# Kernel tuning notes

Hardware: AMD Instinct MI355X
Metric: run time of the kernel (lower is better)

Reference implementation:

```python
import jax, jax.numpy as jnp
import numpy as np

B, D, H, NC = 4096, 128, 4, 10
HD = D // H
EPS = 1e-5


def _ln(x, g, b):
    m = jnp.mean(x, axis=-1, keepdims=True)
    v = jnp.var(x, axis=-1, keepdims=True)
    return (x - m) * jax.lax.rsqrt(v + EPS) * g + b


def _mlp(x, w1, b1, w2, b2):
    h = jax.nn.gelu(x @ w1.T + b1, approximate=False)  # nn.GELU default = exact erf
    return h @ w2.T + b2


def setup_inputs():
    key = jax.random.key(0)
    ks = iter(jax.random.split(key, 40))
    w = lambda *s: jax.random.normal(next(ks), s, dtype=jnp.float32) * 0.02
    inp = {
        'coords': jax.random.uniform(next(ks), (B, 2), dtype=jnp.float32),
        'labels': jax.random.randint(next(ks), (B,), 0, NC),
        'ce_w': w(D, 2), 'ce_b': w(D),
        'emb': w(NC, D),
        'sa_in_w': w(3 * D, D), 'sa_in_b': w(3 * D),
        'sa_out_w': w(D, D), 'sa_out_b': w(D),
        'n1_g': jnp.ones(D), 'n1_b': jnp.zeros(D),
        'm1_w1': w(4 * D, D), 'm1_b1': w(4 * D), 'm1_w2': w(D, 4 * D), 'm1_b2': w(D),
        'n2_g': jnp.ones(D), 'n2_b': jnp.zeros(D),
        'ca_in_w': w(3 * D, D), 'ca_in_b': w(3 * D),
        'ca_out_w': w(D, D), 'ca_out_b': w(D),
        'n3_g': jnp.ones(D), 'n3_b': jnp.zeros(D),
        'm2_w1': w(4 * D, D), 'm2_b1': w(4 * D), 'm2_w2': w(D, 4 * D), 'm2_b2': w(D),
        'n4_g': jnp.ones(D), 'n4_b': jnp.zeros(D),
        'fin_w': w(1, D), 'fin_b': w(1),
    }
    return inp


def reference(coords, labels, ce_w, ce_b, emb, sa_in_w, sa_in_b, sa_out_w, sa_out_b,
              n1_g, n1_b, m1_w1, m1_b1, m1_w2, m1_b2, n2_g, n2_b,
              ca_in_w, ca_in_b, ca_out_w, ca_out_b, n3_g, n3_b,
              m2_w1, m2_b1, m2_w2, m2_b2, n4_g, n4_b, fin_w, fin_b):
    # --- vectorized positional encoding (original loops over batch) ---
    div = 10000.0 ** (2.0 * jnp.arange(D // 2, dtype=jnp.float32) / D)  # [D/2]
    pe_sin = jnp.sin(coords[:, 0:1] / div)  # even slots
    pe_cos = jnp.cos(coords[:, 1:2] / div)  # odd slots
    pe = jnp.stack([pe_sin, pe_cos], axis=-1).reshape(B, D)

    x = coords @ ce_w.T + ce_b + pe  # [B, D]

    # --- self-attention: seq_len = B, batch = 1 (torch seq-first semantics) ---
    qkv = x @ sa_in_w.T + sa_in_b  # [B, 3D]
    q, k, v = jnp.split(qkv, 3, axis=-1)
    q = q.reshape(B, H, HD); k = k.reshape(B, H, HD); v = v.reshape(B, H, HD)
    scores = jnp.einsum('qhd,khd->hqk', q, k) / jnp.sqrt(jnp.float32(HD))  # [H,B,B]
    attn = jax.nn.softmax(scores, axis=-1)
    sa = jnp.einsum('hqk,khd->qhd', attn, v).reshape(B, D) @ sa_out_w.T + sa_out_b

    x = _ln(x + sa, n1_g, n1_b)
    x = _ln(x + _mlp(x, m1_w1, m1_b1, m1_w2, m1_b2), n2_g, n2_b)

    # --- cross-attention: per-sample q_len = kv_len = 1 -> softmax over a
    # single key is exactly 1, so output = out_proj(v_proj(label_emb)) ---
    lab = emb[labels]  # [B, D]
    wv = ca_in_w[2 * D:]; bv = ca_in_b[2 * D:]
    ca = (lab @ wv.T + bv) @ ca_out_w.T + ca_out_b

    x = _ln(x + ca, n3_g, n3_b)
    x = _ln(x + _mlp(x, m2_w1, m2_b1, m2_w2, m2_b2), n4_g, n4_b)

    return jax.nn.sigmoid(x @ fin_w.T + fin_b)  # [B, 1]
```

## Files before the change

### kernel.cpp

```cpp
#include <hip/hip_runtime.h>
#include <hip/hip_bf16.h>


typedef __bf16 bf16_t;
typedef __bf16 bf16x8 __attribute__((ext_vector_type(8)));
typedef __bf16 bf16x4 __attribute__((ext_vector_type(4)));
typedef __bf16 bf16x2 __attribute__((ext_vector_type(2)));
typedef float  f32x4  __attribute__((ext_vector_type(4)));
typedef float  f32x2  __attribute__((ext_vector_type(2)));

__device__ __forceinline__ f32x4 mfma16(bf16x8 a, bf16x8 b, f32x4 c) {
  return __builtin_amdgcn_mfma_f32_16x16x32_bf16(a, b, c, 0, 0, 0);
}

__global__ __launch_bounds__(256) void k_init(const float* __restrict__ coords,
                                              const float* __restrict__ ce_w,
                                              const float* __restrict__ ce_b,
                                              float* __restrict__ xf,
                                              bf16_t* __restrict__ xb,
                                              const float* __restrict__ s0,
                                              const float* __restrict__ s1,
                                              const float* __restrict__ s2,
                                              const float* __restrict__ s3,
                                              const float* __restrict__ s4,
                                              const float* __restrict__ s5,
                                              bf16_t* __restrict__ wdst,
                                              const float* __restrict__ emb,
                                              const float* __restrict__ wvp,
                                              const float* __restrict__ bvp,
                                              const float* __restrict__ cow,
                                              const float* __restrict__ cob,
                                              float* __restrict__ tab) {
  const int bid = blockIdx.x;
  const int tid = threadIdx.x;
  if (bid < 2048) {
    int row = bid * 2 + (tid >> 7);
    int d   = tid & 127;
    float c0 = coords[row * 2 + 0];
    float c1 = coords[row * 2 + 1];
    int   j  = d >> 1;
    float inv = exp2f(-0.20762050593045953f * (float)j);
    float pe  = (d & 1) ? cosf(c1 * inv) : sinf(c0 * inv);
    float x = c0 * ce_w[2 * d] + c1 * ce_w[2 * d + 1] + ce_b[d] + pe;
    xf[(size_t)row * 128 + d] = x;
    xb[(size_t)row * 128 + d] = (bf16_t)x;
  } else if (bid < 2368) {
    int i = (bid - 2048) * 256 + tid;
    const float* src; int off;
    if      (i < 12288) { src = s0; off = i; }
    else if (i < 16384) { src = s1; off = i - 12288; }
    else if (i < 32768) { src = s2; off = i - 16384; }
    else if (i < 49152) { src = s3; off = i - 32768; }
    else if (i < 65536) { src = s4; off = i - 49152; }
    else                { src = s5; off = i - 65536; }
    f32x4 v = *(const f32x4*)(src + (size_t)off * 4);
    bf16x4 o = {(bf16_t)v[0], (bf16_t)v[1], (bf16_t)v[2], (bf16_t)v[3]};
    *(bf16x4*)(wdst + (size_t)i * 4) = o;
  } else {
    __shared__ float embs[10][128];
    __shared__ float t1[10][128];
    for (int i = tid; i < 1280; i += 256) embs[i >> 7][i & 127] = emb[i];
    __syncthreads();
    for (int o = tid; o < 1280; o += 256) {
      int c = o >> 7, n = o & 127;
      float acc = bvp[n];
      const float* wr = wvp + n * 128;
      for (int k2 = 0; k2 < 128; k2++) acc += embs[c][k2] * wr[k2];
      t1[c][n] = acc;
    }
    __syncthreads();
    for (int o = tid; o < 1280; o += 256) {
      int c = o >> 7, dd = o & 127;
      float acc = cob[dd];
      const float* wr = cow + dd * 128;
      for (int n = 0; n < 128; n++) acc += t1[c][n] * wr[n];
      tab[o] = acc;
    }
  }
}

enum { EPI_BF16 = 1, EPI_GELU_BF16 = 2 };

template <int K, int EPI>
__global__ __launch_bounds__(256) void k_gemm(const bf16_t* __restrict__ X,
                                              const bf16_t* __restrict__ Wb,
                                              const float* __restrict__ bias,
                                              bf16_t* __restrict__ outB,
                                              bf16_t* __restrict__ vTout,
                                              int N) {
  const int tid  = threadIdx.x;
  const int lane = tid & 63;
  const int wv   = tid >> 6;
  const int l15  = lane & 15;
  const int quad = lane >> 4;
  const int xbase = blockIdx.x * 64 + (wv >> 1) * 32;
  const int wbase = blockIdx.y * 64 + (wv & 1) * 32;

  const bf16_t* wr0 = Wb + (size_t)(wbase + l15) * K + quad * 8;
  const bf16_t* xr0 = X  + (size_t)(xbase + l15) * K + quad * 8;

  f32x4 acc[2][2];
  const f32x4 zero4 = {0.f, 0.f, 0.f, 0.f};
  for (int i = 0; i < 2; i++)
    for (int t = 0; t < 2; t++) acc[i][t] = zero4;

#pragma unroll 4
  for (int kk = 0; kk < K; kk += 32) {
    bf16x8 a0 = *(const bf16x8*)(wr0 + kk);
    bf16x8 a1 = *(const bf16x8*)(wr0 + 16 * K + kk);
    bf16x8 b0 = *(const bf16x8*)(xr0 + kk);
    bf16x8 b1 = *(const bf16x8*)(xr0 + 16 * K + kk);
    acc[0][0] = mfma16(a0, b0, acc[0][0]);
    acc[0][1] = mfma16(a0, b1, acc[0][1]);
    acc[1][0] = mfma16(a1, b0, acc[1][0]);
    acc[1][1] = mfma16(a1, b1, acc[1][1]);
  }

  f32x4 bv[2];
  bv[0] = *(const f32x4*)(bias + wbase + quad * 4);
  bv[1] = *(const f32x4*)(bias + wbase + 16 + quad * 4);
#pragma unroll
  for (int t = 0; t < 2; t++) {
    int row = xbase + t * 16 + l15;
#pragma unroll
    for (int i = 0; i < 2; i++) {
      int col0 = wbase + i * 16 + quad * 4;
      f32x4 v = acc[i][t] + bv[i];
      if (EPI == EPI_GELU_BF16) {
#pragma unroll
        for (int r = 0; r < 4; r++)
          v[r] = 0.5f * v[r] * (1.0f + erff(v[r] * 0.70710678118654752f));
      }
      bf16x4 o = {(bf16_t)v[0], (bf16_t)v[1], (bf16_t)v[2], (bf16_t)v[3]};
      *(bf16x4*)(outB + (size_t)row * N + col0) = o;
      if (vTout && col0 >= 256) {
#pragma unroll
        for (int r = 0; r < 4; r++)
          vTout[(size_t)(col0 - 256 + r) * 4096 + row] = (bf16_t)v[r];
      }
    }
  }
}

__global__ __launch_bounds__(256, 4) void k_attn(const bf16_t* __restrict__ qkv,
                                                 const bf16_t* __restrict__ vT,
                                                 bf16_t* __restrict__ opart,
                                                 float* __restrict__ lpart) {
  __shared__ bf16_t kbuf[128][36];
  __shared__ bf16_t vbuf[32][136];
  __shared__ bf16_t pt[4][2][16][72];

  const int tid  = threadIdx.x;
  const int lane = tid & 63;
  const int wv   = tid >> 6;
  const int l15  = lane & 15;
  const int quad = lane >> 4;
  const int blk  = blockIdx.x;
  const int h    = blk & 3;
  const int ks   = (blk >> 2) & 7;
  const int qt   = (blk >> 5) * 4 + wv;
  const int q0   = qt * 32;
  const int kb   = ks * 512;
  const int task = (qt * 8 + ks) * 4 + h;

  bf16x8 qfA, qfB;
  {
    bf16x8 ra = *(const bf16x8*)(qkv + (size_t)(q0 + l15) * 384 + h * 32 + quad * 8);
    bf16x8 rb = *(const bf16x8*)(qkv + (size_t)(q0 + 16 + l15) * 384 + h * 32 + quad * 8);
#pragma unroll
    for (int j = 0; j < 8; j++) {
      qfA[j] = (bf16_t)((float)ra[j] * 0.17677669529663687f);
      qfB[j] = (bf16_t)((float)rb[j] * 0.17677669529663687f);
    }
  }

  const f32x4 zero4 = {0.f, 0.f, 0.f, 0.f};
  f32x4 oA0 = zero4, oA1 = zero4, oB0 = zero4, oB1 = zero4;
  float laccA = 0.f, laccB = 0.f;

  for (int kk = 0; kk < 512; kk += 128) {
    __syncthreads();
#pragma unroll
    for (int rep = 0; rep < 2; rep++) {
      int idx = rep * 256 + tid;
      int row = idx >> 2, seg = idx & 3;
      bf16x8 t8 = *(const bf16x8*)(qkv + (size_t)(kb + kk + row) * 384
                                   + 128 + h * 32 + seg * 8);
      *(bf16x8*)&kbuf[row][seg * 8] = t8;
      int dim = idx >> 4, vseg = idx & 15;
      bf16x8 v8 = *(const bf16x8*)(vT + (size_t)(h * 32 + dim) * 4096
                                   + kb + kk + vseg * 8);
      *(bf16x8*)&vbuf[dim][vseg * 8] = v8;
    }
    __syncthreads();

#pragma unroll
    for (int half = 0; half < 2; half++) {
      const int ko = half * 64;
      bf16x8 kf0 = *(const bf16x8*)&kbuf[ko + l15][quad * 8];
      bf16x8 kf1 = *(const bf16x8*)&kbuf[ko + 16 + l15][quad * 8];
      bf16x8 kf2 = *(const bf16x8*)&kbuf[ko + 32 + l15][quad * 8];
      bf16x8 kf3 = *(const bf16x8*)&kbuf[ko + 48 + l15][quad * 8];

      f32x4 sA[4], sB[4];
      sA[0] = mfma16(kf0, qfA, zero4);
      sA[1] = mfma16(kf1, qfA, zero4);
      sA[2] = mfma16(kf2, qfA, zero4);
      sA[3] = mfma16(kf3, qfA, zero4);
      sB[0] = mfma16(kf0, qfB, zero4);
      sB[1] = mfma16(kf1, qfB, zero4);
      sB[2] = mfma16(kf2, qfB, zero4);
      sB[3] = mfma16(kf3, qfB, zero4);

#pragma unroll
      for (int t = 0; t < 4; t++) {
        float a0 = __expf(sA[t][0]), a1 = __expf(sA[t][1]);
        float a2 = __expf(sA[t][2]), a3 = __expf(sA[t][3]);
        laccA += (a0 + a1) + (a2 + a3);
        bf16x4 pa = {(bf16_t)a0, (bf16_t)a1, (bf16_t)a2, (bf16_t)a3};
        *(bf16x4*)&pt[wv][0][l15][t * 16 + quad * 4] = pa;
        float b0 = __expf(sB[t][0]), b1 = __expf(sB[t][1]);
        float b2 = __expf(sB[t][2]), b3 = __expf(sB[t][3]);
        laccB += (b0 + b1) + (b2 + b3);
        bf16x4 pb = {(bf16_t)b0, (bf16_t)b1, (bf16_t)b2, (bf16_t)b3};
        *(bf16x4*)&pt[wv][1][l15][t * 16 + quad * 4] = pb;
      }

      bf16x8 pA0 = *(const bf16x8*)&pt[wv][0][l15][quad * 8];
      bf16x8 pA1 = *(const bf16x8*)&pt[wv][0][l15][32 + quad * 8];
      bf16x8 pB0 = *(const bf16x8*)&pt[wv][1][l15][quad * 8];
      bf16x8 pB1 = *(const bf16x8*)&pt[wv][1][l15][32 + quad * 8];

      bf16x8 v00 = *(const bf16x8*)&vbuf[l15][ko + quad * 8];
      bf16x8 v01 = *(const bf16x8*)&vbuf[16 + l15][ko + quad * 8];
      bf16x8 v10 = *(const bf16x8*)&vbuf[l15][ko + 32 + quad * 8];
      bf16x8 v11 = *(const bf16x8*)&vbuf[16 + l15][ko + 32 + quad * 8];

      oA0 = mfma16(pA0, v00, oA0);
      oA0 = mfma16(pA1, v10, oA0);
      oA1 = mfma16(pA0, v01, oA1);
      oA1 = mfma16(pA1, v11, oA1);
      oB0 = mfma16(pB0, v00, oB0);
      oB0 = mfma16(pB1, v10, oB0);
      oB1 = mfma16(pB0, v01, oB1);
      oB1 = mfma16(pB1, v11, oB1);
    }
  }

  laccA += __shfl_xor(laccA, 16, 64); laccA += __shfl_xor(laccA, 32, 64);
  laccB += __shfl_xor(laccB, 16, 64); laccB += __shfl_xor(laccB, 32, 64);
  if (quad == 0) {
    lpart[task * 32 + l15]      = laccA;
    lpart[task * 32 + 16 + l15] = laccB;
  }

  size_t ob = (size_t)task * 1024;
#pragma unroll
  for (int r = 0; r < 4; r++) {
    int qa = quad * 4 + r;
    opart[ob + qa * 32 + l15]             = (bf16_t)oA0[r];
    opart[ob + qa * 32 + 16 + l15]        = (bf16_t)oA1[r];
    opart[ob + (16 + qa) * 32 + l15]      = (bf16_t)oB0[r];
    opart[ob + (16 + qa) * 32 + 16 + l15] = (bf16_t)oB1[r];
  }
}

__global__ __launch_bounds__(256) void k_attn_fin(const bf16_t* __restrict__ opart,
                                                  const float* __restrict__ lpart,
                                                  bf16_t* __restrict__ attnb) {
  int idx = blockIdx.x * 256 + threadIdx.x;
  int d  = idx & 31;
  int q  = (idx >> 5) & 4095;
  int h  = idx >> 17;
  int qt = q >> 5, ql = q & 31;
  float O = 0.f, L = 0.f;
#pragma unroll
  for (int ks = 0; ks < 8; ks++) {
    int t = (qt * 8 + ks) * 4 + h;
    O += (float)opart[(size_t)t * 1024 + ql * 32 + d];
    L += lpart[t * 32 + ql];
  }
  attnb[(size_t)q * 128 + h * 32 + d] = (bf16_t)(O / L);
}

__global__ __launch_bounds__(512) void k_tail(
    const bf16_t* __restrict__ attnb, const float* __restrict__ xf,
    const bf16_t* __restrict__ wso, const float* __restrict__ bso,
    const float* __restrict__ n1g, const float* __restrict__ n1b,
    const bf16_t* __restrict__ w11, const float* __restrict__ b11,
    const bf16_t* __restrict__ w12, const float* __restrict__ b12,
    const float* __restrict__ n2g, const float* __restrict__ n2b,
    const int* __restrict__ labels, const float* __restrict__ tab,
    const float* __restrict__ n3g, const float* __restrict__ n3b,
    const bf16_t* __restrict__ w21, const float* __restrict__ b21,
    const bf16_t* __restrict__ w22, const float* __restrict__ b22,
    const float* __restrict__ n4g, const float* __restrict__ n4b,
    const float* __restrict__ fw, const float* __restrict__ fb,
    float* __restrict__ out) {
  __shared__ float  xs[16][132];
  __shared__ bf16_t xsb[16][136];
  __shared__ bf16_t hb[16][520];
  __shared__ float  red[2][16][8];

  const int tid  = threadIdx.x;
  const int lane = tid & 63;
  const int wv   = tid >> 6;
  const int l15  = lane & 15;
  const int quad = lane >> 4;
  const int row  = blockIdx.x * 16 + l15;
  const int cb1  = wv * 16;
  const int c1   = cb1 + quad * 4;
  const int cb4  = wv * 64;

  const f32x4 zero4 = {0.f, 0.f, 0.f, 0.f};

  {
    f32x4 acc = zero4;
    const bf16_t* br = attnb + (size_t)row * 128 + quad * 8;
    const bf16_t* ar = wso + (size_t)(cb1 + l15) * 128 + quad * 8;
#pragma unroll
    for (int kk = 0; kk < 128; kk += 32)
      acc = mfma16(*(const bf16x8*)(ar + kk), *(const bf16x8*)(br + kk), acc);

    f32x4 v = acc + *(const f32x4*)(bso + c1)
                  + *(const f32x4*)(xf + (size_t)row * 128 + c1);
    float s  = (v[0] + v[1]) + (v[2] + v[3]);
    float sq = (v[0]*v[0] + v[1]*v[1]) + (v[2]*v[2] + v[3]*v[3]);
    s  += __shfl_xor(s, 16, 64);  s  += __shfl_xor(s, 32, 64);
    sq += __shfl_xor(sq, 16, 64); sq += __shfl_xor(sq, 32, 64);
    if (quad == 0) { red[0][l15][wv] = s; red[1][l15][wv] = sq; }
    __syncthreads();
    float S = 0.f, SQ = 0.f;
#pragma unroll
    for (int w2 = 0; w2 < 8; w2++) { S += red[0][l15][w2]; SQ += red[1][l15][w2]; }
    float mean = S * (1.f / 128.f);
    float rstd = rsqrtf(SQ * (1.f / 128.f) - mean * mean + 1e-5f);
    f32x4 y = (v - mean) * rstd * (*(const f32x4*)(n1g + c1))
            + *(const f32x4*)(n1b + c1);
    *(f32x4*)&xs[l15][c1] = y;
    bf16x4 o = {(bf16_t)y[0], (bf16_t)y[1], (bf16_t)y[2], (bf16_t)y[3]};
    *(bf16x4*)&xsb[l15][c1] = o;
  }
  __syncthreads();

  {
    f32x4 au[4] = {zero4, zero4, zero4, zero4};
#pragma unroll
    for (int kk = 0; kk < 128; kk += 32) {
      bf16x8 bfr = *(const bf16x8*)&xsb[l15][kk + quad * 8];
#pragma unroll
      for (int i = 0; i < 4; i++) {
        bf16x8 a = *(const bf16x8*)(w11 + (size_t)(cb4 + i * 16 + l15) * 128
                                    + kk + quad * 8);
        au[i] = mfma16(a, bfr, au[i]);
      }
    }
#pragma unroll
    for (int i = 0; i < 4; i++) {
      int c = cb4 + i * 16 + quad * 4;
      f32x4 vv = au[i] + *(const f32x4*)(b11 + c);
#pragma unroll
      for (int r = 0; r < 4; r++)
        vv[r] = 0.5f * vv[r] * (1.0f + erff(vv[r] * 0.70710678118654752f));
      bf16x4 o = {(bf16_t)vv[0], (bf16_t)vv[1], (bf16_t)vv[2], (bf16_t)vv[3]};
      *(bf16x4*)&hb[l15][c] = o;
    }
  }
  __syncthreads();

  {
    f32x4 acc = zero4;
    const bf16_t* ar = w12 + (size_t)(cb1 + l15) * 512 + quad * 8;
#pragma unroll 4
    for (int kk = 0; kk < 512; kk += 32) {
      bf16x8 bfr = *(const bf16x8*)&hb[l15][kk + quad * 8];
      acc = mfma16(*(const bf16x8*)(ar + kk), bfr, acc);
    }
    f32x4 v = acc + *(const f32x4*)(b12 + c1) + *(const f32x4*)&xs[l15][c1];
    float s  = (v[0] + v[1]) + (v[2] + v[3]);
    float sq = (v[0]*v[0] + v[1]*v[1]) + (v[2]*v[2] + v[3]*v[3]);
    s  += __shfl_xor(s, 16, 64);  s  += __shfl_xor(s, 32, 64);
    sq += __shfl_xor(sq, 16, 64); sq += __shfl_xor(sq, 32, 64);
    if (quad == 0) { red[0][l15][wv] = s; red[1][l15][wv] = sq; }
    __syncthreads();
    float S = 0.f, SQ = 0.f;
#pragma unroll
    for (int w2 = 0; w2 < 8; w2++) { S += red[0][l15][w2]; SQ += red[1][l15][w2]; }
    float mean = S * (1.f / 128.f);
    float rstd = rsqrtf(SQ * (1.f / 128.f) - mean * mean + 1e-5f);
    int lab = labels[row];
    f32x4 y = (v - mean) * rstd * (*(const f32x4*)(n2g + c1))
            + *(const f32x4*)(n2b + c1)
            + *(const f32x4*)(tab + (size_t)lab * 128 + c1);
    float s3  = (y[0] + y[1]) + (y[2] + y[3]);
    float sq3 = (y[0]*y[0] + y[1]*y[1]) + (y[2]*y[2] + y[3]*y[3]);
    s3  += __shfl_xor(s3, 16, 64);  s3  += __shfl_xor(s3, 32, 64);
    sq3 += __shfl_xor(sq3, 16, 64); sq3 += __shfl_xor(sq3, 32, 64);
    __syncthreads();
    if (quad == 0) { red[0][l15][wv] = s3; red[1][l15][wv] = sq3; }
    __syncthreads();
    float S3 = 0.f, SQ3 = 0.f;
#pragma unroll
    for (int w2 = 0; w2 < 8; w2++) { S3 += red[0][l15][w2]; SQ3 += red[1][l15][w2]; }
    float mean3 = S3 * (1.f / 128.f);
    float rstd3 = rsqrtf(SQ3 * (1.f / 128.f) - mean3 * mean3 + 1e-5f);
    f32x4 y3 = (y - mean3) * rstd3 * (*(const f32x4*)(n3g + c1))
             + *(const f32x4*)(n3b + c1);
    *(f32x4*)&xs[l15][c1] = y3;
    bf16x4 o = {(bf16_t)y3[0], (bf16_t)y3[1], (bf16_t)y3[2], (bf16_t)y3[3]};
    *(bf16x4*)&xsb[l15][c1] = o;
  }
  __syncthreads();

  {
    f32x4 au[4] = {zero4, zero4, zero4, zero4};
#pragma unroll
    for (int kk = 0; kk < 128; kk += 32) {
      bf16x8 bfr = *(const bf16x8*)&xsb[l15][kk + quad * 8];
#pragma unroll
      for (int i = 0; i < 4; i++) {
        bf16x8 a = *(const bf16x8*)(w21 + (size_t)(cb4 + i * 16 + l15) * 128
                                    + kk + quad * 8);
        au[i] = mfma16(a, bfr, au[i]);
      }
    }
#pragma unroll
    for (int i = 0; i < 4; i++) {
      int c = cb4 + i * 16 + quad * 4;
      f32x4 vv = au[i] + *(const f32x4*)(b21 + c);
#pragma unroll
      for (int r = 0; r < 4; r++)
        vv[r] = 0.5f * vv[r] * (1.0f + erff(vv[r] * 0.70710678118654752f));
      bf16x4 o = {(bf16_t)vv[0], (bf16_t)vv[1], (bf16_t)vv[2], (bf16_t)vv[3]};
      *(bf16x4*)&hb[l15][c] = o;
    }
  }
  __syncthreads();

  {
    f32x4 acc = zero4;
    const bf16_t* ar = w22 + (size_t)(cb1 + l15) * 512 + quad * 8;
#pragma unroll 4
    for (int kk = 0; kk < 512; kk += 32) {
      bf16x8 bfr = *(const bf16x8*)&hb[l15][kk + quad * 8];
      acc = mfma16(*(const bf16x8*)(ar + kk), bfr, acc);
    }
    f32x4 v = acc + *(const f32x4*)(b22 + c1) + *(const f32x4*)&xs[l15][c1];
    float s  = (v[0] + v[1]) + (v[2] + v[3]);
    float sq = (v[0]*v[0] + v[1]*v[1]) + (v[2]*v[2] + v[3]*v[3]);
    s  += __shfl_xor(s, 16, 64);  s  += __shfl_xor(s, 32, 64);
    sq += __shfl_xor(sq, 16, 64); sq += __shfl_xor(sq, 32, 64);
    if (quad == 0) { red[0][l15][wv] = s; red[1][l15][wv] = sq; }
    __syncthreads();
    float S = 0.f, SQ = 0.f;
#pragma unroll
    for (int w2 = 0; w2 < 8; w2++) { S += red[0][l15][w2]; SQ += red[1][l15][w2]; }
    float mean = S * (1.f / 128.f);
    float rstd = rsqrtf(SQ * (1.f / 128.f) - mean * mean + 1e-5f);
    f32x4 y = (v - mean) * rstd * (*(const f32x4*)(n4g + c1))
            + *(const f32x4*)(n4b + c1);
    f32x4 fwv = *(const f32x4*)(fw + c1);
    float dot = (y[0]*fwv[0] + y[1]*fwv[1]) + (y[2]*fwv[2] + y[3]*fwv[3]);
    dot += __shfl_xor(dot, 16, 64); dot += __shfl_xor(dot, 32, 64);
    __syncthreads();
    if (quad == 0) red[0][l15][wv] = dot;
    __syncthreads();
    if (wv == 0 && quad == 0) {
      float logit = fb[0];
#pragma unroll
      for (int w2 = 0; w2 < 8; w2++) logit += red[0][l15][w2];
      out[row] = 1.0f / (1.0f + expf(-logit));
    }
  }
}

extern "C" void kernel_launch(void* const* d_in, const int* in_sizes, int n_in,
                              void* d_out, int out_size, void* d_ws, size_t ws_size,
                              hipStream_t stream) {
  const float* coords  = (const float*)d_in[0];
  const int*   labels  = (const int*)d_in[1];
  const float* ce_w    = (const float*)d_in[2];
  const float* ce_b    = (const float*)d_in[3];
  const float* emb     = (const float*)d_in[4];
  const float* sa_in_w = (const float*)d_in[5];
  const float* sa_in_b = (const float*)d_in[6];
  const float* sa_out_w= (const float*)d_in[7];
  const float* sa_out_b= (const float*)d_in[8];
  const float* n1_g    = (const float*)d_in[9];
  const float* n1_b    = (const float*)d_in[10];
  const float* m1_w1   = (const float*)d_in[11];
  const float* m1_b1   = (const float*)d_in[12];
  const float* m1_w2   = (const float*)d_in[13];
  const float* m1_b2   = (const float*)d_in[14];
  const float* n2_g    = (const float*)d_in[15];
  const float* n2_b    = (const float*)d_in[16];
  const float* ca_in_w = (const float*)d_in[17];
  const float* ca_in_b = (const float*)d_in[18];
  const float* ca_out_w= (const float*)d_in[19];
  const float* ca_out_b= (const float*)d_in[20];
  const float* n3_g    = (const float*)d_in[21];
  const float* n3_b    = (const float*)d_in[22];
  const float* m2_w1   = (const float*)d_in[23];
  const float* m2_b1   = (const float*)d_in[24];
  const float* m2_w2   = (const float*)d_in[25];
  const float* m2_b2   = (const float*)d_in[26];
  const float* n4_g    = (const float*)d_in[27];
  const float* n4_b    = (const float*)d_in[28];
  const float* fin_w   = (const float*)d_in[29];
  const float* fin_b   = (const float*)d_in[30];
  float* outp = (float*)d_out;

  char* w = (char*)d_ws;
  float*  xf    = (float*)(w);
  float*  tab   = (float*)(w + 2097152);
  bf16_t* wsb   = (bf16_t*)(w + 2105344);
  bf16_t* xb    = (bf16_t*)(w + 2760704);
  bf16_t* attnb = (bf16_t*)(w + 3809280);
  bf16_t* qkvb  = (bf16_t*)(w + 4857856);
  bf16_t* vT    = (bf16_t*)(w + 8003584);
  bf16_t* opart = (bf16_t*)(w + 9052160);
  float*  lpart = (float*)(w + 17440768);

  bf16_t* w_sain  = wsb;
  bf16_t* w_saout = wsb + 49152;
  bf16_t* w_m1w1  = wsb + 65536;
  bf16_t* w_m1w2  = wsb + 131072;
  bf16_t* w_m2w1  = wsb + 196608;
  bf16_t* w_m2w2  = wsb + 262144;

  k_init<<<2369, 256, 0, stream>>>(coords, ce_w, ce_b, xf, xb,
                                   sa_in_w, sa_out_w, m1_w1, m1_w2, m2_w1, m2_w2,
                                   wsb, emb, ca_in_w + 256 * 128, ca_in_b + 256,
                                   ca_out_w, ca_out_b, tab);
  k_gemm<128, EPI_BF16><<<dim3(64, 6), 256, 0, stream>>>(xb, w_sain, sa_in_b,
                                                         qkvb, vT, 384);
  k_attn<<<1024, 256, 0, stream>>>(qkvb, vT, opart, lpart);
  k_attn_fin<<<2048, 256, 0, stream>>>(opart, lpart, attnb);
  k_tail<<<256, 512, 0, stream>>>(attnb, xf,
                                  w_saout, sa_out_b, n1_g, n1_b,
                                  w_m1w1, m1_b1, w_m1w2, m1_b2, n2_g, n2_b,
                                  labels, tab, n3_g, n3_b,
                                  w_m2w1, m2_b1, w_m2w2, m2_b2, n4_g, n4_b,
                                  fin_w, fin_b, outp);

  (void)in_sizes; (void)n_in; (void)out_size; (void)ws_size;
}
```

Before: 192.6 us.

## Fuse attention split-K reduction into tail kernel and compact init kernel

Removes the separate k_attn_fin launch: the tail kernel now sums the eight key-split partial outputs and normalisers per row into shared memory and feeds them directly to the out-projection MFMA. This drops one kernel launch and the attnb round-trip through global memory. k_init is reshaped to 257 blocks of 512 threads, each thread handling four embedding columns with vector stores and also doing the weight bf16 conversion. The QKV GEMM is specialised with fixed K and N and a fully unrolled loop. The tail kernel gains extra shared memory and a serial reduction prologue, which may lower its occupancy.

```diff
diff --git a/kernel.cpp b/kernel.cpp
--- a/kernel.cpp
+++ b/kernel.cpp
@@ -5,15 +5,13 @@
 typedef __bf16 bf16_t;
 typedef __bf16 bf16x8 __attribute__((ext_vector_type(8)));
 typedef __bf16 bf16x4 __attribute__((ext_vector_type(4)));
-typedef __bf16 bf16x2 __attribute__((ext_vector_type(2)));
 typedef float  f32x4  __attribute__((ext_vector_type(4)));
-typedef float  f32x2  __attribute__((ext_vector_type(2)));
 
 __device__ __forceinline__ f32x4 mfma16(bf16x8 a, bf16x8 b, f32x4 c) {
   return __builtin_amdgcn_mfma_f32_16x16x32_bf16(a, b, c, 0, 0, 0);
 }
 
-__global__ __launch_bounds__(256) void k_init(const float* __restrict__ coords,
+__global__ __launch_bounds__(512) void k_init(const float* __restrict__ coords,
                                               const float* __restrict__ ce_w,
                                               const float* __restrict__ ce_b,
                                               float* __restrict__ xf,
@@ -31,63 +29,65 @@
                                               const float* __restrict__ cow,
                                               const float* __restrict__ cob,
                                               float* __restrict__ tab) {
+  __shared__ float embs[10][128];
+  __shared__ float t1[10][128];
   const int bid = blockIdx.x;
   const int tid = threadIdx.x;
-  if (bid < 2048) {
-    int row = bid * 2 + (tid >> 7);
-    int d   = tid & 127;
+  if (bid < 256) {
+    int c = bid * 512 + tid;
+    int row = c >> 5, d0 = (c & 31) * 4;
     float c0 = coords[row * 2 + 0];
     float c1 = coords[row * 2 + 1];
-    int   j  = d >> 1;
-    float inv = exp2f(-0.20762050593045953f * (float)j);
-    float pe  = (d & 1) ? cosf(c1 * inv) : sinf(c0 * inv);
-    float x = c0 * ce_w[2 * d] + c1 * ce_w[2 * d + 1] + ce_b[d] + pe;
-    xf[(size_t)row * 128 + d] = x;
-    xb[(size_t)row * 128 + d] = (bf16_t)x;
-  } else if (bid < 2368) {
-    int i = (bid - 2048) * 256 + tid;
-    const float* src; int off;
-    if      (i < 12288) { src = s0; off = i; }
-    else if (i < 16384) { src = s1; off = i - 12288; }
-    else if (i < 32768) { src = s2; off = i - 16384; }
-    else if (i < 49152) { src = s3; off = i - 32768; }
-    else if (i < 65536) { src = s4; off = i - 49152; }
-    else                { src = s5; off = i - 65536; }
-    f32x4 v = *(const f32x4*)(src + (size_t)off * 4);
-    bf16x4 o = {(bf16_t)v[0], (bf16_t)v[1], (bf16_t)v[2], (bf16_t)v[3]};
-    *(bf16x4*)(wdst + (size_t)i * 4) = o;
+    f32x4 xv; bf16x4 xo;
+#pragma unroll
+    for (int r = 0; r < 4; r++) {
+      int d = d0 + r, j = d >> 1;
+      float inv = exp2f(-0.20762050593045953f * (float)j);
+      float pe  = (d & 1) ? cosf(c1 * inv) : sinf(c0 * inv);
+      float x = c0 * ce_w[2 * d] + c1 * ce_w[2 * d + 1] + ce_b[d] + pe;
+      xv[r] = x; xo[r] = (bf16_t)x;
+    }
+    *(f32x4*)(xf + (size_t)row * 128 + d0) = xv;
+    *(bf16x4*)(xb + (size_t)row * 128 + d0) = xo;
+
+    if (c < 81920) {
+      const float* src; int off;
+      if      (c < 12288) { src = s0; off = c; }
+      else if (c < 16384) { src = s1; off = c - 12288; }
+      else if (c < 32768) { src = s2; off = c - 16384; }
+      else if (c < 49152) { src = s3; off = c - 32768; }
+      else if (c < 65536) { src = s4; off = c - 49152; }
+      else                { src = s5; off = c - 65536; }
+      f32x4 v = *(const f32x4*)(src + (size_t)off * 4);
+      bf16x4 o = {(bf16_t)v[0], (bf16_t)v[1], (bf16_t)v[2], (bf16_t)v[3]};
+      *(bf16x4*)(wdst + (size_t)c * 4) = o;
+    }
   } else {
-    __shared__ float embs[10][128];
-    __shared__ float t1[10][128];
-    for (int i = tid; i < 1280; i += 256) embs[i >> 7][i & 127] = emb[i];
-    __syncthreads();
-    for (int o = tid; o < 1280; o += 256) {
-      int c = o >> 7, n = o & 127;
+    for (int i = tid; i < 1280; i += 512) embs[i >> 7][i & 127] = emb[i];
+    __syncthreads();
+    for (int o = tid; o < 1280; o += 512) {
+      int cc = o >> 7, n = o & 127;
       float acc = bvp[n];
       const float* wr = wvp + n * 128;
-      for (int k2 = 0; k2 < 128; k2++) acc += embs[c][k2] * wr[k2];
-      t1[c][n] = acc;
-    }
-    __syncthreads();
-    for (int o = tid; o < 1280; o += 256) {
-      int c = o >> 7, dd = o & 127;
+      for (int k2 = 0; k2 < 128; k2++) acc += embs[cc][k2] * wr[k2];
+      t1[cc][n] = acc;
+    }
+    __syncthreads();
+    for (int o = tid; o < 1280; o += 512) {
+      int cc = o >> 7, dd = o & 127;
       float acc = cob[dd];
       const float* wr = cow + dd * 128;
-      for (int n = 0; n < 128; n++) acc += t1[c][n] * wr[n];
+      for (int n = 0; n < 128; n++) acc += t1[cc][n] * wr[n];
       tab[o] = acc;
     }
   }
 }
 
-enum { EPI_BF16 = 1, EPI_GELU_BF16 = 2 };
-
-template <int K, int EPI>
-__global__ __launch_bounds__(256) void k_gemm(const bf16_t* __restrict__ X,
-                                              const bf16_t* __restrict__ Wb,
-                                              const float* __restrict__ bias,
-                                              bf16_t* __restrict__ outB,
-                                              bf16_t* __restrict__ vTout,
-                                              int N) {
+__global__ __launch_bounds__(256) void k_gemm_qkv(const bf16_t* __restrict__ X,
+                                                  const bf16_t* __restrict__ Wb,
+                                                  const float* __restrict__ bias,
+                                                  bf16_t* __restrict__ outB,
+                                                  bf16_t* __restrict__ vTout) {
   const int tid  = threadIdx.x;
   const int lane = tid & 63;
   const int wv   = tid >> 6;
@@ -96,20 +96,20 @@
   const int xbase = blockIdx.x * 64 + (wv >> 1) * 32;
   const int wbase = blockIdx.y * 64 + (wv & 1) * 32;
 
-  const bf16_t* wr0 = Wb + (size_t)(wbase + l15) * K + quad * 8;
-  const bf16_t* xr0 = X  + (size_t)(xbase + l15) * K + quad * 8;
+  const bf16_t* wr0 = Wb + (size_t)(wbase + l15) * 128 + quad * 8;
+  const bf16_t* xr0 = X  + (size_t)(xbase + l15) * 128 + quad * 8;
 
   f32x4 acc[2][2];
   const f32x4 zero4 = {0.f, 0.f, 0.f, 0.f};
   for (int i = 0; i < 2; i++)
     for (int t = 0; t < 2; t++) acc[i][t] = zero4;
 
-#pragma unroll 4
-  for (int kk = 0; kk < K; kk += 32) {
+#pragma unroll
+  for (int kk = 0; kk < 128; kk += 32) {
     bf16x8 a0 = *(const bf16x8*)(wr0 + kk);
-    bf16x8 a1 = *(const bf16x8*)(wr0 + 16 * K + kk);
+    bf16x8 a1 = *(const bf16x8*)(wr0 + 16 * 128 + kk);
     bf16x8 b0 = *(const bf16x8*)(xr0 + kk);
-    bf16x8 b1 = *(const bf16x8*)(xr0 + 16 * K + kk);
+    bf16x8 b1 = *(const bf16x8*)(xr0 + 16 * 128 + kk);
     acc[0][0] = mfma16(a0, b0, acc[0][0]);
     acc[0][1] = mfma16(a0, b1, acc[0][1]);
     acc[1][0] = mfma16(a1, b0, acc[1][0]);
@@ -126,14 +126,9 @@
     for (int i = 0; i < 2; i++) {
       int col0 = wbase + i * 16 + quad * 4;
       f32x4 v = acc[i][t] + bv[i];
-      if (EPI == EPI_GELU_BF16) {
-#pragma unroll
-        for (int r = 0; r < 4; r++)
-          v[r] = 0.5f * v[r] * (1.0f + erff(v[r] * 0.70710678118654752f));
-      }
       bf16x4 o = {(bf16_t)v[0], (bf16_t)v[1], (bf16_t)v[2], (bf16_t)v[3]};
-      *(bf16x4*)(outB + (size_t)row * N + col0) = o;
-      if (vTout && col0 >= 256) {
+      *(bf16x4*)(outB + (size_t)row * 384 + col0) = o;
+      if (col0 >= 256) {
 #pragma unroll
         for (int r = 0; r < 4; r++)
           vTout[(size_t)(col0 - 256 + r) * 4096 + row] = (bf16_t)v[r];
@@ -265,26 +260,9 @@
   }
 }
 
-__global__ __launch_bounds__(256) void k_attn_fin(const bf16_t* __restrict__ opart,
-                                                  const float* __restrict__ lpart,
-                                                  bf16_t* __restrict__ attnb) {
-  int idx = blockIdx.x * 256 + threadIdx.x;
-  int d  = idx & 31;
-  int q  = (idx >> 5) & 4095;
-  int h  = idx >> 17;
-  int qt = q >> 5, ql = q & 31;
-  float O = 0.f, L = 0.f;
-#pragma unroll
-  for (int ks = 0; ks < 8; ks++) {
-    int t = (qt * 8 + ks) * 4 + h;
-    O += (float)opart[(size_t)t * 1024 + ql * 32 + d];
-    L += lpart[t * 32 + ql];
-  }
-  attnb[(size_t)q * 128 + h * 32 + d] = (bf16_t)(O / L);
-}
-
 __global__ __launch_bounds__(512) void k_tail(
-    const bf16_t* __restrict__ attnb, const float* __restrict__ xf,
+    const bf16_t* __restrict__ opart, const float* __restrict__ lpart,
+    const float* __restrict__ xf,
     const bf16_t* __restrict__ wso, const float* __restrict__ bso,
     const float* __restrict__ n1g, const float* __restrict__ n1b,
     const bf16_t* __restrict__ w11, const float* __restrict__ b11,
@@ -299,29 +277,54 @@
     float* __restrict__ out) {
   __shared__ float  xs[16][132];
   __shared__ bf16_t xsb[16][136];
+  __shared__ bf16_t att[16][136];
   __shared__ bf16_t hb[16][520];
   __shared__ float  red[2][16][8];
-
+  __shared__ float  Ls[16][4];
+
+  const int b    = blockIdx.x;
   const int tid  = threadIdx.x;
   const int lane = tid & 63;
   const int wv   = tid >> 6;
   const int l15  = lane & 15;
   const int quad = lane >> 4;
-  const int row  = blockIdx.x * 16 + l15;
+  const int row  = b * 16 + l15;
   const int cb1  = wv * 16;
   const int c1   = cb1 + quad * 4;
   const int cb4  = wv * 64;
 
   const f32x4 zero4 = {0.f, 0.f, 0.f, 0.f};
 
+  if (tid < 64) {
+    int rr = tid >> 2, hh = tid & 3;
+    int q = b * 16 + rr, qt = q >> 5, ql = q & 31;
+    float L = 0.f;
+#pragma unroll
+    for (int ks = 0; ks < 8; ks++) L += lpart[((qt * 8 + ks) * 4 + hh) * 32 + ql];
+    Ls[rr][hh] = L;
+  }
+  __syncthreads();
+#pragma unroll
+  for (int r = 0; r < 4; r++) {
+    int idx = r * 512 + tid;
+    int rr = idx >> 7, d = idx & 127, hh = d >> 5, dd = d & 31;
+    int q = b * 16 + rr, qt = q >> 5, ql = q & 31;
+    float O = 0.f;
+#pragma unroll
+    for (int ks = 0; ks < 8; ks++)
+      O += (float)opart[(size_t)((qt * 8 + ks) * 4 + hh) * 1024 + ql * 32 + dd];
+    att[rr][d] = (bf16_t)(O / Ls[rr][hh]);
+  }
+  __syncthreads();
+
   {
     f32x4 acc = zero4;
-    const bf16_t* br = attnb + (size_t)row * 128 + quad * 8;
     const bf16_t* ar = wso + (size_t)(cb1 + l15) * 128 + quad * 8;
 #pragma unroll
-    for (int kk = 0; kk < 128; kk += 32)
-      acc = mfma16(*(const bf16x8*)(ar + kk), *(const bf16x8*)(br + kk), acc);
-
+    for (int kk = 0; kk < 128; kk += 32) {
+      bf16x8 bfr = *(const bf16x8*)&att[l15][kk + quad * 8];
+      acc = mfma16(*(const bf16x8*)(ar + kk), bfr, acc);
+    }
     f32x4 v = acc + *(const f32x4*)(bso + c1)
                   + *(const f32x4*)(xf + (size_t)row * 128 + c1);
     float s  = (v[0] + v[1]) + (v[2] + v[3]);
@@ -515,7 +518,6 @@
   float*  tab   = (float*)(w + 2097152);
   bf16_t* wsb   = (bf16_t*)(w + 2105344);
   bf16_t* xb    = (bf16_t*)(w + 2760704);
-  bf16_t* attnb = (bf16_t*)(w + 3809280);
   bf16_t* qkvb  = (bf16_t*)(w + 4857856);
   bf16_t* vT    = (bf16_t*)(w + 8003584);
   bf16_t* opart = (bf16_t*)(w + 9052160);
@@ -528,15 +530,13 @@
   bf16_t* w_m2w1  = wsb + 196608;
   bf16_t* w_m2w2  = wsb + 262144;
 
-  k_init<<<2369, 256, 0, stream>>>(coords, ce_w, ce_b, xf, xb,
-                                   sa_in_w, sa_out_w, m1_w1, m1_w2, m2_w1, m2_w2,
-                                   wsb, emb, ca_in_w + 256 * 128, ca_in_b + 256,
-                                   ca_out_w, ca_out_b, tab);
-  k_gemm<128, EPI_BF16><<<dim3(64, 6), 256, 0, stream>>>(xb, w_sain, sa_in_b,
-                                                         qkvb, vT, 384);
+  k_init<<<257, 512, 0, stream>>>(coords, ce_w, ce_b, xf, xb,
+                                  sa_in_w, sa_out_w, m1_w1, m1_w2, m2_w1, m2_w2,
+                                  wsb, emb, ca_in_w + 256 * 128, ca_in_b + 256,
+                                  ca_out_w, ca_out_b, tab);
+  k_gemm_qkv<<<dim3(64, 6), 256, 0, stream>>>(xb, w_sain, sa_in_b, qkvb, vT);
   k_attn<<<1024, 256, 0, stream>>>(qkvb, vT, opart, lpart);
-  k_attn_fin<<<2048, 256, 0, stream>>>(opart, lpart, attnb);
-  k_tail<<<256, 512, 0, stream>>>(attnb, xf,
+  k_tail<<<256, 512, 0, stream>>>(opart, lpart, xf,
                                   w_saout, sa_out_b, n1_g, n1_b,
                                   w_m1w1, m1_b1, w_m1w2, m1_b2, n2_g, n2_b,
                                   labels, tab, n3_g, n3_b,
```

New measurement: 187.3 us (median of 2 runs). 1.03x faster.
